# Kernel tuning notes

Measured on AMD Instinct MI355X. Metric: run time of the kernel, lower is better.

## Reference

```python
import jax, jax.numpy as jnp
import numpy as np

H_DIM = 256
N_HEADS = 8
HALF = H_DIM // 2

def _lin(x, W, b):
    # torch nn.Linear: y = x @ W.T + b
    y = x @ W.T
    return y + b if b is not None else y

def setup_inputs() -> dict:
    key = jax.random.key(0)
    ks = jax.random.split(key, 16)
    s = 0.02
    d = {
        'x': jax.random.normal(ks[0], (16, H_DIM, 32, 32), jnp.float32),
        'q1_w': jax.random.normal(ks[1], (HALF, HALF), jnp.float32) * s,
        'q1_b': jnp.zeros((HALF,), jnp.float32),
        'q2_w': jax.random.normal(ks[2], (HALF, HALF), jnp.float32) * s,
        'q2_b': jnp.zeros((HALF,), jnp.float32),
        'k1_w': jax.random.normal(ks[3], (HALF, HALF), jnp.float32) * s,
        'k1_b': jnp.zeros((HALF,), jnp.float32),
        'k2_w': jax.random.normal(ks[4], (HALF, HALF), jnp.float32) * s,
        'k2_b': jnp.zeros((HALF,), jnp.float32),
        'v1_w': jax.random.normal(ks[5], (HALF, HALF), jnp.float32) * s,
        'v1_b': jnp.zeros((HALF,), jnp.float32),
        'v2_w': jax.random.normal(ks[6], (HALF, HALF), jnp.float32) * s,
        'v2_b': jnp.zeros((HALF,), jnp.float32),
        'proj1_w': jax.random.normal(ks[7], (HALF, HALF), jnp.float32) * s,
        'proj1_b': jnp.zeros((HALF,), jnp.float32),
        'proj2_w': jax.random.normal(ks[8], (HALF, HALF), jnp.float32) * s,
        'proj2_b': jnp.zeros((HALF,), jnp.float32),
        'logit_scale': jnp.log(10.0 * jnp.ones((N_HEADS, 1, 1), jnp.float32)),
        'mlp_w1': jax.random.normal(ks[9], (128, 2), jnp.float32) * s,
        'mlp_b1': jnp.zeros((128,), jnp.float32),
        'mlp_w2': jax.random.normal(ks[10], (N_HEADS, 128), jnp.float32) * s,
    }
    return d

def _rel_pos_index(h, w):
    # static (numpy) relative position index, shape [N, N]
    ch, cw = np.meshgrid(np.arange(h), np.arange(w), indexing='ij')
    coords = np.stack([ch.reshape(-1), cw.reshape(-1)])  # [2, N]
    rel = coords[:, :, None] - coords[:, None, :]         # [2, N, N]
    rel = rel.transpose(1, 2, 0)
    rel[:, :, 0] += h - 1
    rel[:, :, 1] += w - 1
    return rel[:, :, 0] * (2 * w - 1) + rel[:, :, 1]

def _forward(x, q1_w, q1_b, q2_w, q2_b, k1_w, k1_b, k2_w, k2_b,
             v1_w, v1_b, v2_w, v2_b, proj1_w, proj1_b, proj2_w, proj2_b,
             logit_scale, mlp_w1, mlp_b1, mlp_w2):
    b, c, h, w = x.shape
    N = h * w
    nh = N_HEADS
    hd = c // nh
    x3 = jnp.transpose(x, (0, 2, 3, 1)).reshape(b, N, c)
    x0, x1 = x3[..., :c // 2], x3[..., c // 2:]

    def qkv(W0, b0, W1, b1):
        t = jnp.concatenate([x0 + _lin(x0, W0, b0), x1 + _lin(x1, W1, b1)], axis=-1)
        return t.reshape(b, N, nh, hd).transpose(0, 2, 1, 3)  # [b, nh, N, hd]

    q = qkv(q1_w, q1_b, q2_w, q2_b)
    k = qkv(k1_w, k1_b, k2_w, k2_b)
    v = qkv(v1_w, v1_b, v2_w, v2_b)

    eps = 1e-12
    qn = q / jnp.maximum(jnp.linalg.norm(q, axis=-1, keepdims=True), eps)
    kn = k / jnp.maximum(jnp.linalg.norm(k, axis=-1, keepdims=True), eps)
    attn = jnp.einsum('bhnd,bhmd->bhnm', qn, kn)  # cosine similarity
    scale = jnp.exp(jnp.minimum(logit_scale, jnp.log(1.0 / 0.01)))  # [nh,1,1]
    attn = attn * scale[None]

    # continuous relative-position bias (CPB) table via small MLP
    rch = jnp.arange(-(h - 1), h, dtype=jnp.float32) / (h - 1 + 1e-8)
    rcw = jnp.arange(-(w - 1), w, dtype=jnp.float32) / (w - 1 + 1e-8)
    gh, gw = jnp.meshgrid(rch, rcw, indexing='ij')
    tab = jnp.stack([gh, gw], axis=-1) * 3.2               # [2h-1, 2w-1, 2]
    tab = jnp.sign(tab) * (1.0 - jnp.exp(-jnp.abs(tab)))
    tab = jax.nn.relu(_lin(tab, mlp_w1, mlp_b1))
    tab = _lin(tab, mlp_w2, None).reshape(-1, nh)          # [(2h-1)(2w-1), nh]

    idx = jnp.asarray(_rel_pos_index(h, w))                # [N, N]
    bias = tab[idx.reshape(-1)].reshape(N, N, nh).transpose(2, 0, 1)
    bias = 16.0 * jax.nn.sigmoid(bias)
    attn = attn + bias[None]

    attn = jax.nn.softmax(attn, axis=-1)
    out = jnp.einsum('bhnm,bhmd->bhnd', attn, v).transpose(0, 2, 1, 3).reshape(b, N, c)
    o0, o1 = out[..., :c // 2], out[..., c // 2:]
    out = jnp.concatenate([_lin(o0, proj1_w, proj1_b), _lin(o1, proj2_w, proj2_b)], axis=-1)
    return out.reshape(b, h, w, c).transpose(0, 3, 1, 2)

def reference(x, q1_w, q1_b, q2_w, q2_b, k1_w, k1_b, k2_w, k2_b,
              v1_w, v1_b, v2_w, v2_b, proj1_w, proj1_b, proj2_w, proj2_b,
              logit_scale, mlp_w1, mlp_b1, mlp_w2):
    return _forward(x, q1_w, q1_b, q2_w, q2_b, k1_w, k1_b, k2_w, k2_b,
                    v1_w, v1_b, v2_w, v2_b, proj1_w, proj1_b, proj2_w, proj2_b,
                    logit_scale, mlp_w1, mlp_b1, mlp_w2)
```

## Files before the change

kernel.cpp:

```cpp
#include <hip/hip_runtime.h>
#include <cmath>


typedef _Float16 half_t;
typedef __attribute__((ext_vector_type(2))) __fp16 fp16x2;
typedef __attribute__((ext_vector_type(4))) _Float16 half4;
typedef __attribute__((ext_vector_type(8))) _Float16 half8;
typedef __attribute__((ext_vector_type(2))) float float2v;
typedef __attribute__((ext_vector_type(4))) float float4v;
typedef __attribute__((ext_vector_type(4))) unsigned int uint4v;

static __device__ __forceinline__ float4v mfma16(half8 a, half8 b, float4v c) {
  return __builtin_amdgcn_mfma_f32_16x16x32_f16(a, b, c, 0, 0, 0);
}

struct PtrArr8 { const float* p[8]; };

__global__ __launch_bounds__(256) void prep_all(
    PtrArr8 wsrc, PtrArr8 bsrc, half_t* __restrict__ wf,
    float* __restrict__ bws, const float* __restrict__ w1,
    const float* __restrict__ b1, const float* __restrict__ w2,
    const float* __restrict__ ls, float* __restrict__ tabd) {
  __shared__ float smem[1408];
  int blk = blockIdx.x;
  int t = threadIdx.x;
  if (blk < 128) {
    int y = blk >> 4, xx = blk & 15;
    const float* src = nullptr;
    const float* bs = nullptr;
#pragma unroll
    for (int i = 0; i < 8; i++)
      if (i == y) { src = wsrc.p[i]; bs = bsrc.p[i]; }
    int flat = (xx * 256 + t) * 4;
    float4 w = *(const float4*)(src + flat);
    int j = flat >> 7, k = flat & 127;
    if (y < 6) {
      if (k == j)     w.x += 1.0f;
      if (k + 1 == j) w.y += 1.0f;
      if (k + 2 == j) w.z += 1.0f;
      if (k + 3 == j) w.w += 1.0f;
    }
    half4 h;
    h[0] = (half_t)w.x;
    h[1] = (half_t)w.y;
    h[2] = (half_t)w.z;
    h[3] = (half_t)w.w;
    int ng = j >> 4, l = j & 15, ks = k >> 5, quad = (k >> 3) & 3, o8 = k & 7;
    *(half4*)(wf + y * 16384 + ((ng * 4 + ks) * 64 + quad * 16 + l) * 8 +
              o8) = h;
    if (xx == 0 && t < 128) bws[y * 128 + t] = bs[t];
  } else {
    float* sw1 = smem;
    float* sb1 = smem + 256;
    float* sw2 = smem + 384;
    sw1[t] = w1[t];
    if (t < 128) sb1[t] = b1[t];
    for (int i = t; i < 1024; i += 256) sw2[i] = w2[i];
    __syncthreads();
    int p = (blk - 128) * 256 + t;
    if (p >= 3969) return;
    int ph = p / 63, pw = p % 63;
    float t0 = (float)(ph - 31) * (3.2f / 31.0f);
    float t1 = (float)(pw - 31) * (3.2f / 31.0f);
    t0 = copysignf(1.0f - __expf(-fabsf(t0)), t0);
    t1 = copysignf(1.0f - __expf(-fabsf(t1)), t1);
    float acc[8];
#pragma unroll
    for (int hh = 0; hh < 8; hh++) acc[hh] = 0.0f;
    for (int j = 0; j < 128; j++) {
      float hj = fmaxf(0.0f, t0 * sw1[2 * j] + t1 * sw1[2 * j + 1] + sb1[j]);
#pragma unroll
      for (int hh = 0; hh < 8; hh++) acc[hh] += hj * sw2[hh * 128 + j];
    }
    const float L2E = 1.44269504f;
#pragma unroll
    for (int hh = 0; hh < 8; hh++) {
      float scale = __expf(fminf(ls[hh], 4.6051702f));
      float c14 = 14.0f - (scale + 16.0f) * L2E;
      float bias = 16.0f / (1.0f + __expf(-acc[hh]));
      float v = bias * L2E + c14;
      float* td = tabd + hh * 7940;
      td[p * 2 + 1] = v;
      td[p * 2 + 2] = v;
      if (p == 0) td[0] = 0.0f;
    }
  }
}

__global__ __launch_bounds__(256, 4) void qkv_mfma(
    const float* __restrict__ x, const half_t* __restrict__ wfrag,
    const float* __restrict__ lscale, const float* __restrict__ bws,
    half_t* __restrict__ qf, half_t* __restrict__ kf,
    half_t* __restrict__ vf) {
  __shared__ half_t tbuf[4608];
  int t = threadIdx.x;
  int lane = t & 63, wv = t >> 6, l = lane & 15, quad = lane >> 4;
  int rw = wv & 1, cw = wv >> 1;
  int hf = blockIdx.y;
  int m0 = blockIdx.x * 32;
  int b = m0 >> 10, n0 = m0 & 1023;

  {
    const float* xb = x + ((size_t)b * 256 + hf * 128) * 1024 + n0;
    int ch = t >> 3, no = (t & 7) * 4;
#pragma unroll
    for (int p = 0; p < 4; p++) {
      float4 v = *(const float4*)(xb + (size_t)(p * 32 + ch) * 1024 + no);
      half4 h;
      h[0] = (half_t)v.x;
      h[1] = (half_t)v.y;
      h[2] = (half_t)v.z;
      h[3] = (half_t)v.w;
      *(half4*)(tbuf + (p * 32 + ch) * 36 + no) = h;
    }
  }
  __syncthreads();

  half8 afr[4];
#pragma unroll
  for (int ks = 0; ks < 4; ks++) {
    half8 a;
#pragma unroll
    for (int j = 0; j < 8; j++)
      a[j] = tbuf[(ks * 32 + quad * 8 + j) * 36 + rw * 16 + l];
    afr[ks] = a;
  }
  __syncthreads();

  for (int op = 0; op < 3; op++) {
    int combo = op * 2 + hf;
    const half_t* wfb = wfrag + combo * 16384;
    float4v acc[4];
#pragma unroll
    for (int ngl = 0; ngl < 4; ngl++) {
      int ng = cw * 4 + ngl;
      float4v c = {0.f, 0.f, 0.f, 0.f};
#pragma unroll
      for (int ks = 0; ks < 4; ks++) {
        half8 bfrag =
            *(const half8*)(wfb + ((ng * 4 + ks) * 64 + lane) * 8);
        c = mfma16(afr[ks], bfrag, c);
      }
      acc[ngl] = c;
    }
#pragma unroll
    for (int ngl = 0; ngl < 4; ngl++) {
      float bb = bws[combo * 128 + (cw * 4 + ngl) * 16 + l];
#pragma unroll
      for (int r2 = 0; r2 < 4; r2++) acc[ngl][r2] += bb;
    }
    if (op < 2) {
#pragma unroll
      for (int hgl = 0; hgl < 2; hgl++) {
        float sc = 1.0f;
        if (op == 0)
          sc = __expf(fminf(lscale[hf * 4 + cw * 2 + hgl], 4.6051702f)) *
               1.44269504f;
#pragma unroll
        for (int r2 = 0; r2 < 4; r2++) {
          float ss = acc[2 * hgl][r2] * acc[2 * hgl][r2] +
                     acc[2 * hgl + 1][r2] * acc[2 * hgl + 1][r2];
          ss += __shfl_xor(ss, 1, 64);
          ss += __shfl_xor(ss, 2, 64);
          ss += __shfl_xor(ss, 4, 64);
          ss += __shfl_xor(ss, 8, 64);
          float rn = sc / fmaxf(sqrtf(ss), 1e-12f);
          acc[2 * hgl][r2] *= rn;
          acc[2 * hgl + 1][r2] *= rn;
        }
      }
#pragma unroll
      for (int ngl = 0; ngl < 4; ngl++)
#pragma unroll
        for (int r2 = 0; r2 < 4; r2++)
          tbuf[(rw * 16 + quad * 4 + r2) * 136 + (cw * 4 + ngl) * 16 + l] =
              (half_t)acc[ngl][r2];
      __syncthreads();
      half_t* dst = (op == 0) ? qf : kf;
#pragma unroll
      for (int i = 0; i < 2; i++) {
        int idx = t + 256 * i;
        int row = idx >> 4, colc = (idx & 15) * 8;
        half8 vv = *(const half8*)(tbuf + row * 136 + colc);
        int head = hf * 4 + (colc >> 5), d = colc & 31;
        *(half8*)(dst + (((size_t)b * 8 + head) * 1024 + n0 + row) * 32 + d) =
            vv;
      }
      __syncthreads();
    } else {
#pragma unroll
      for (int ngl = 0; ngl < 4; ngl++) {
        int col = (cw * 4 + ngl) * 16 + l;
        half4 hv;
#pragma unroll
        for (int r2 = 0; r2 < 4; r2++) hv[r2] = (half_t)acc[ngl][r2];
        *(half4*)(tbuf + col * 36 + rw * 16 + quad * 4) = hv;
      }
      __syncthreads();
      int p64 = (n0 >> 5) & 1;
      int nb64 = n0 & ~63;
#pragma unroll
      for (int i = 0; i < 8; i++) {
        int idx = t + 256 * i;
        int col = idx >> 4, rp = idx & 15;
        unsigned int val = *(const unsigned int*)(tbuf + col * 36 + rp * 2);
        int head = hf * 4 + (col >> 5);
        int d = col & 31;
        int npos = nb64 + ((rp >> 1) & 3) * 16 + (rp & 1) * 8 + p64 * 4 +
                   ((rp >> 3) & 1) * 2;
        *(unsigned int*)((char*)vf +
                         (((((size_t)b * 8 + head) * 32 + d) * 1024) + npos) *
                             2) = val;
      }
    }
  }
}


#define LOADK(kt)                                                           \
  {                                                                         \
    _Pragma("unroll") for (int nt = 0; nt < 4; nt++)                        \
        kfr[nt] = *(const half8*)(kbase + ((kt)*64 + nt * 16 + l) * 32 +    \
                                  quad * 8);                                \
  }

#define LOADV(kt)                                                           \
  {                                                                         \
    _Pragma("unroll") for (int ks = 0; ks < 2; ks++) {                      \
      vv0[ks] = *(const half8*)(vbase + l * 1024 + (kt)*64 + quad * 16 +    \
                                ks * 8);                                    \
      vv1[ks] = *(const half8*)(vbase + (16 + l) * 1024 + (kt)*64 +         \
                                quad * 16 + ks * 8);                        \
    }                                                                       \
  }

#define QK_PHASE(kt, S, SR)                                                 \
  {                                                                         \
    int rowb = (wv + 31 - 2 * (kt)) * 63 + cA + (S)*16;                     \
    _Pragma("unroll") for (int nt = 0; nt < 4; nt++) {                      \
      int base = rowb - (nt >> 1) * 63 - (nt & 1) * 16;                     \
      float2v p0 = sb2d[base];                                              \
      float2v p1 = sb2d[base - 2];                                          \
      float4v c;                                                            \
      c[0] = p0[1];                                                         \
      c[1] = p0[0];                                                         \
      c[2] = p1[1];                                                         \
      c[3] = p1[0];                                                         \
      SR[nt] = mfma16(kfr[nt], qfr[S], c);                                  \
    }                                                                       \
  }

#define EXP_PACK(S, SR)                                                     \
  {                                                                         \
    unsigned int w0[4], w1[4];                                              \
    _Pragma("unroll") for (int nt = 0; nt < 4; nt++) {                      \
      fp16x2 plo = __builtin_amdgcn_cvt_pkrtz(                              \
          __builtin_amdgcn_exp2f(SR[nt][0]),                                \
          __builtin_amdgcn_exp2f(SR[nt][1]));                               \
      fp16x2 phi = __builtin_amdgcn_cvt_pkrtz(                              \
          __builtin_amdgcn_exp2f(SR[nt][2]),                                \
          __builtin_amdgcn_exp2f(SR[nt][3]));                               \
      w0[nt] = __builtin_bit_cast(unsigned int, plo);                       \
      w1[nt] = __builtin_bit_cast(unsigned int, phi);                       \
    }                                                                       \
    uint4v u0 = {w0[0], w0[1], w0[2], w0[3]};                               \
    uint4v u1 = {w1[0], w1[1], w1[2], w1[3]};                               \
    pf##S[0] = __builtin_bit_cast(half8, u0);                               \
    pf##S[1] = __builtin_bit_cast(half8, u1);                               \
  }

#define PV_PHASE(S)                                                         \
  {                                                                         \
    _Pragma("unroll") for (int ks = 0; ks < 2; ks++) {                      \
      o0[S] = mfma16(pf##S[ks], vv0[ks], o0[S]);                            \
      o1[S] = mfma16(pf##S[ks], vv1[ks], o1[S]);                            \
      accl[S] = mfma16(pf##S[ks], ones, accl[S]);                           \
    }                                                                       \
  }

__global__ __launch_bounds__(256) void attn_mfma(
    const half_t* __restrict__ qf, const half_t* __restrict__ kf,
    const half_t* __restrict__ vf, const float* __restrict__ tabd,
    half_t* __restrict__ ao) {
  __shared__ float2v sb2d[2205];

  int id = blockIdx.x;
  int qo = id >> 7;
  int bh = id & 127;
  int h = bh & 7, b = bh >> 3;
  int t = threadIdx.x;
  int lane = t & 63, wv = t >> 6, l = lane & 15, quad = lane >> 4;
  size_t bhs = (size_t)b * 8 + h;
  const half_t* kbase = kf + bhs * 1024 * 32;
  const half_t* vbase = vf + bhs * 32 * 1024;
  int row0 = qo * 128 + wv * 32;
  int cA = l + 31 - quad * 4;

  half8 kfr[4], vv0[2], vv1[2], qfr[2], pf0[2], pf1[2];
  LOADK(0);
  LOADV(0);
#pragma unroll
  for (int s = 0; s < 2; s++)
    qfr[s] = *(const half8*)(qf + (bhs * 1024 + row0 + s * 16 + l) * 32 +
                             quad * 8);

  {
    const float2v* td =
        (const float2v*)(tabd + (size_t)h * 7940) + qo * 252;
    for (int i = t; i < 2205; i += 256) sb2d[i] = td[i];
  }

  float4v o0[2], o1[2], accl[2];
#pragma unroll
  for (int s = 0; s < 2; s++) {
    o0[s] = (float4v){0.f, 0.f, 0.f, 0.f};
    o1[s] = (float4v){0.f, 0.f, 0.f, 0.f};
    accl[s] = (float4v){0.f, 0.f, 0.f, 0.f};
  }
  half8 ones;
#pragma unroll
  for (int j = 0; j < 8; j++) ones[j] = (half_t)1.0f;

  __syncthreads();

#pragma unroll
  for (int kt = 0; kt < 16; ++kt) {
    float4v sres[4];
    QK_PHASE(kt, 0, sres);
    EXP_PACK(0, sres);
    float4v sres2[4];
    QK_PHASE(kt, 1, sres2);
    if (kt < 15) LOADK(kt + 1);
    EXP_PACK(1, sres2);
    PV_PHASE(0);
    PV_PHASE(1);
    if (kt < 15) LOADV(kt + 1);
  }

#pragma unroll
  for (int s = 0; s < 2; s++) {
#pragma unroll
    for (int r2 = 0; r2 < 4; r2++) {
      float linv = 1.0f / accl[s][r2];
      size_t rowaddr =
          ((size_t)b * 1024 + row0 + s * 16 + quad * 4 + r2) * 256 + h * 32;
      ao[rowaddr + l] = (half_t)(o0[s][r2] * linv);
      ao[rowaddr + 16 + l] = (half_t)(o1[s][r2] * linv);
    }
  }
}

__global__ __launch_bounds__(256, 4) void proj_mfma(
    const half_t* __restrict__ ao, const half_t* __restrict__ wfrag,
    const float* __restrict__ bws, float* __restrict__ out) {
  __shared__ float yt[128 * 36];
  int t = threadIdx.x;
  int lane = t & 63, wv = t >> 6, l = lane & 15, quad = lane >> 4;
  int rw = wv & 1, cw = wv >> 1;
  int hf = blockIdx.y;
  int m0 = blockIdx.x * 32;
  int b = m0 >> 10, n0 = m0 & 1023;

  half8 afr[4];
  const half_t* ab =
      ao + ((size_t)m0 + rw * 16 + l) * 256 + hf * 128 + quad * 8;
#pragma unroll
  for (int ks = 0; ks < 4; ks++) afr[ks] = *(const half8*)(ab + ks * 32);

  const half_t* wfb = wfrag + (6 + hf) * 16384;
#pragma unroll
  for (int ngl = 0; ngl < 4; ngl++) {
    int ng = cw * 4 + ngl;
    float4v c = {0.f, 0.f, 0.f, 0.f};
#pragma unroll
    for (int ks = 0; ks < 4; ks++) {
      half8 bfrag = *(const half8*)(wfb + ((ng * 4 + ks) * 64 + lane) * 8);
      c = mfma16(afr[ks], bfrag, c);
    }
    float bb = bws[(6 + hf) * 128 + ng * 16 + l];
#pragma unroll
    for (int r2 = 0; r2 < 4; r2++) c[r2] += bb;
    *(float4v*)(yt + (ng * 16 + l) * 36 + rw * 16 + quad * 4) = c;
  }
  __syncthreads();
#pragma unroll
  for (int i = 0; i < 4; i++) {
    int idx = t + 256 * i;
    int col = idx >> 3, rg = idx & 7;
    float4v vv = *(const float4v*)(yt + col * 36 + rg * 4);
    *(float4v*)(out + ((size_t)b * 256 + hf * 128 + col) * 1024 + n0 +
                rg * 4) = vv;
  }
}

extern "C" void kernel_launch(void* const* d_in, const int* in_sizes, int n_in,
                              void* d_out, int out_size, void* d_ws,
                              size_t ws_size, hipStream_t stream) {
  (void)in_sizes; (void)n_in; (void)out_size; (void)ws_size;
  const float* x = (const float*)d_in[0];

  half_t* ws = (half_t*)d_ws;
  half_t* qfp = ws;
  half_t* kfp = ws + 4194304;
  half_t* vfp = ws + 8388608;
  half_t* aop = ws + 12582912;
  half_t* wfp = ws + 16777216;
  float* tabd = (float*)((char*)d_ws + 33816576);
  float* bws = (float*)((char*)d_ws + 34070656);

  PtrArr8 wsrc, bsrc;
  const int widx[8] = {1, 3, 5, 7, 9, 11, 13, 15};
  for (int i = 0; i < 8; i++) {
    wsrc.p[i] = (const float*)d_in[widx[i]];
    bsrc.p[i] = (const float*)d_in[widx[i] + 1];
  }

  prep_all<<<144, 256, 0, stream>>>(wsrc, bsrc, wfp, bws,
                                    (const float*)d_in[18],
                                    (const float*)d_in[19],
                                    (const float*)d_in[20],
                                    (const float*)d_in[17], tabd);
  qkv_mfma<<<dim3(512, 2), 256, 0, stream>>>(x, wfp, (const float*)d_in[17],
                                             bws, qfp, kfp, vfp);
  attn_mfma<<<1024, 256, 0, stream>>>(qfp, kfp, vfp, tabd, aop);
  proj_mfma<<<dim3(512, 2), 256, 0, stream>>>(aop, wfp, bws, (float*)d_out);
}
```

Baseline: 189.9 us.

## Fuse all four kernels into one persistent kernel with grid barriers

Merges the weight/bias-table prep, QKV projection, attention and output projection kernels into one 1024-block kernel that separates the stages with software grid-wide barriers built on atomic counters. A memset resets the barrier counter before each launch. The aim is to remove three kernel-launch gaps and their tail effects. It depends on all 1024 blocks being resident at once (256 CUs × 4 blocks), otherwise it deadlocks, and it adds barrier spin time plus the cost of the memset.

After: 702.8 us. 270% more time.

```diff
diff --git a/kernel.cpp b/kernel.cpp
--- a/kernel.cpp
+++ b/kernel.cpp
@@ -14,208 +14,47 @@
   return __builtin_amdgcn_mfma_f32_16x16x32_f16(a, b, c, 0, 0, 0);
 }
 
-struct PtrArr8 { const float* p[8]; };
-
-__global__ __launch_bounds__(256) void prep_all(
-    PtrArr8 wsrc, PtrArr8 bsrc, half_t* __restrict__ wf,
-    float* __restrict__ bws, const float* __restrict__ w1,
-    const float* __restrict__ b1, const float* __restrict__ w2,
-    const float* __restrict__ ls, float* __restrict__ tabd) {
-  __shared__ float smem[1408];
-  int blk = blockIdx.x;
-  int t = threadIdx.x;
-  if (blk < 128) {
-    int y = blk >> 4, xx = blk & 15;
-    const float* src = nullptr;
-    const float* bs = nullptr;
-#pragma unroll
-    for (int i = 0; i < 8; i++)
-      if (i == y) { src = wsrc.p[i]; bs = bsrc.p[i]; }
-    int flat = (xx * 256 + t) * 4;
-    float4 w = *(const float4*)(src + flat);
-    int j = flat >> 7, k = flat & 127;
-    if (y < 6) {
-      if (k == j)     w.x += 1.0f;
-      if (k + 1 == j) w.y += 1.0f;
-      if (k + 2 == j) w.z += 1.0f;
-      if (k + 3 == j) w.w += 1.0f;
-    }
-    half4 h;
-    h[0] = (half_t)w.x;
-    h[1] = (half_t)w.y;
-    h[2] = (half_t)w.z;
-    h[3] = (half_t)w.w;
-    int ng = j >> 4, l = j & 15, ks = k >> 5, quad = (k >> 3) & 3, o8 = k & 7;
-    *(half4*)(wf + y * 16384 + ((ng * 4 + ks) * 64 + quad * 16 + l) * 8 +
-              o8) = h;
-    if (xx == 0 && t < 128) bws[y * 128 + t] = bs[t];
-  } else {
-    float* sw1 = smem;
-    float* sb1 = smem + 256;
-    float* sw2 = smem + 384;
-    sw1[t] = w1[t];
-    if (t < 128) sb1[t] = b1[t];
-    for (int i = t; i < 1024; i += 256) sw2[i] = w2[i];
-    __syncthreads();
-    int p = (blk - 128) * 256 + t;
-    if (p >= 3969) return;
-    int ph = p / 63, pw = p % 63;
-    float t0 = (float)(ph - 31) * (3.2f / 31.0f);
-    float t1 = (float)(pw - 31) * (3.2f / 31.0f);
-    t0 = copysignf(1.0f - __expf(-fabsf(t0)), t0);
-    t1 = copysignf(1.0f - __expf(-fabsf(t1)), t1);
-    float acc[8];
-#pragma unroll
-    for (int hh = 0; hh < 8; hh++) acc[hh] = 0.0f;
-    for (int j = 0; j < 128; j++) {
-      float hj = fmaxf(0.0f, t0 * sw1[2 * j] + t1 * sw1[2 * j + 1] + sb1[j]);
-#pragma unroll
-      for (int hh = 0; hh < 8; hh++) acc[hh] += hj * sw2[hh * 128 + j];
-    }
-    const float L2E = 1.44269504f;
-#pragma unroll
-    for (int hh = 0; hh < 8; hh++) {
-      float scale = __expf(fminf(ls[hh], 4.6051702f));
-      float c14 = 14.0f - (scale + 16.0f) * L2E;
-      float bias = 16.0f / (1.0f + __expf(-acc[hh]));
-      float v = bias * L2E + c14;
-      float* td = tabd + hh * 7940;
-      td[p * 2 + 1] = v;
-      td[p * 2 + 2] = v;
-      if (p == 0) td[0] = 0.0f;
-    }
-  }
+struct FusedArgs {
+  const float* x;
+  const float* wsrc[8];
+  const float* bsrc[8];
+  const float* w1;
+  const float* b1;
+  const float* w2;
+  const float* ls;
+  half_t* wf;
+  float* bws;
+  float* tabd;
+  half_t* qf;
+  half_t* kf;
+  half_t* vf;
+  half_t* ao;
+  float* out;
+  unsigned* bar;
+};
+
+static __device__ __forceinline__ void grid_barrier(unsigned* cnt,
+                                                    unsigned* gen,
+                                                    unsigned nb) {
+  __syncthreads();
+  if (threadIdx.x == 0) {
+    unsigned g =
+        __hip_atomic_load(gen, __ATOMIC_RELAXED, __HIP_MEMORY_SCOPE_AGENT);
+    unsigned prev = __hip_atomic_fetch_add(cnt, 1u, __ATOMIC_ACQ_REL,
+                                           __HIP_MEMORY_SCOPE_AGENT);
+    if (prev == nb - 1u) {
+      __hip_atomic_store(cnt, 0u, __ATOMIC_RELAXED,
+                         __HIP_MEMORY_SCOPE_AGENT);
+      __hip_atomic_fetch_add(gen, 1u, __ATOMIC_ACQ_REL,
+                             __HIP_MEMORY_SCOPE_AGENT);
+    } else {
+      while (__hip_atomic_load(gen, __ATOMIC_ACQUIRE,
+                               __HIP_MEMORY_SCOPE_AGENT) == g)
+        __builtin_amdgcn_s_sleep(8);
+    }
+  }
+  __syncthreads();
 }
-
-__global__ __launch_bounds__(256, 4) void qkv_mfma(
-    const float* __restrict__ x, const half_t* __restrict__ wfrag,
-    const float* __restrict__ lscale, const float* __restrict__ bws,
-    half_t* __restrict__ qf, half_t* __restrict__ kf,
-    half_t* __restrict__ vf) {
-  __shared__ half_t tbuf[4608];
-  int t = threadIdx.x;
-  int lane = t & 63, wv = t >> 6, l = lane & 15, quad = lane >> 4;
-  int rw = wv & 1, cw = wv >> 1;
-  int hf = blockIdx.y;
-  int m0 = blockIdx.x * 32;
-  int b = m0 >> 10, n0 = m0 & 1023;
-
-  {
-    const float* xb = x + ((size_t)b * 256 + hf * 128) * 1024 + n0;
-    int ch = t >> 3, no = (t & 7) * 4;
-#pragma unroll
-    for (int p = 0; p < 4; p++) {
-      float4 v = *(const float4*)(xb + (size_t)(p * 32 + ch) * 1024 + no);
-      half4 h;
-      h[0] = (half_t)v.x;
-      h[1] = (half_t)v.y;
-      h[2] = (half_t)v.z;
-      h[3] = (half_t)v.w;
-      *(half4*)(tbuf + (p * 32 + ch) * 36 + no) = h;
-    }
-  }
-  __syncthreads();
-
-  half8 afr[4];
-#pragma unroll
-  for (int ks = 0; ks < 4; ks++) {
-    half8 a;
-#pragma unroll
-    for (int j = 0; j < 8; j++)
-      a[j] = tbuf[(ks * 32 + quad * 8 + j) * 36 + rw * 16 + l];
-    afr[ks] = a;
-  }
-  __syncthreads();
-
-  for (int op = 0; op < 3; op++) {
-    int combo = op * 2 + hf;
-    const half_t* wfb = wfrag + combo * 16384;
-    float4v acc[4];
-#pragma unroll
-    for (int ngl = 0; ngl < 4; ngl++) {
-      int ng = cw * 4 + ngl;
-      float4v c = {0.f, 0.f, 0.f, 0.f};
-#pragma unroll
-      for (int ks = 0; ks < 4; ks++) {
-        half8 bfrag =
-            *(const half8*)(wfb + ((ng * 4 + ks) * 64 + lane) * 8);
-        c = mfma16(afr[ks], bfrag, c);
-      }
-      acc[ngl] = c;
-    }
-#pragma unroll
-    for (int ngl = 0; ngl < 4; ngl++) {
-      float bb = bws[combo * 128 + (cw * 4 + ngl) * 16 + l];
-#pragma unroll
-      for (int r2 = 0; r2 < 4; r2++) acc[ngl][r2] += bb;
-    }
-    if (op < 2) {
-#pragma unroll
-      for (int hgl = 0; hgl < 2; hgl++) {
-        float sc = 1.0f;
-        if (op == 0)
-          sc = __expf(fminf(lscale[hf * 4 + cw * 2 + hgl], 4.6051702f)) *
-               1.44269504f;
-#pragma unroll
-        for (int r2 = 0; r2 < 4; r2++) {
-          float ss = acc[2 * hgl][r2] * acc[2 * hgl][r2] +
-                     acc[2 * hgl + 1][r2] * acc[2 * hgl + 1][r2];
-          ss += __shfl_xor(ss, 1, 64);
-          ss += __shfl_xor(ss, 2, 64);
-          ss += __shfl_xor(ss, 4, 64);
-          ss += __shfl_xor(ss, 8, 64);
-          float rn = sc / fmaxf(sqrtf(ss), 1e-12f);
-          acc[2 * hgl][r2] *= rn;
-          acc[2 * hgl + 1][r2] *= rn;
-        }
-      }
-#pragma unroll
-      for (int ngl = 0; ngl < 4; ngl++)
-#pragma unroll
-        for (int r2 = 0; r2 < 4; r2++)
-          tbuf[(rw * 16 + quad * 4 + r2) * 136 + (cw * 4 + ngl) * 16 + l] =
-              (half_t)acc[ngl][r2];
-      __syncthreads();
-      half_t* dst = (op == 0) ? qf : kf;
-#pragma unroll
-      for (int i = 0; i < 2; i++) {
-        int idx = t + 256 * i;
-        int row = idx >> 4, colc = (idx & 15) * 8;
-        half8 vv = *(const half8*)(tbuf + row * 136 + colc);
-        int head = hf * 4 + (colc >> 5), d = colc & 31;
-        *(half8*)(dst + (((size_t)b * 8 + head) * 1024 + n0 + row) * 32 + d) =
-            vv;
-      }
-      __syncthreads();
-    } else {
-#pragma unroll
-      for (int ngl = 0; ngl < 4; ngl++) {
-        int col = (cw * 4 + ngl) * 16 + l;
-        half4 hv;
-#pragma unroll
-        for (int r2 = 0; r2 < 4; r2++) hv[r2] = (half_t)acc[ngl][r2];
-        *(half4*)(tbuf + col * 36 + rw * 16 + quad * 4) = hv;
-      }
-      __syncthreads();
-      int p64 = (n0 >> 5) & 1;
-      int nb64 = n0 & ~63;
-#pragma unroll
-      for (int i = 0; i < 8; i++) {
-        int idx = t + 256 * i;
-        int col = idx >> 4, rp = idx & 15;
-        unsigned int val = *(const unsigned int*)(tbuf + col * 36 + rp * 2);
-        int head = hf * 4 + (col >> 5);
-        int d = col & 31;
-        int npos = nb64 + ((rp >> 1) & 3) * 16 + (rp & 1) * 8 + p64 * 4 +
-                   ((rp >> 3) & 1) * 2;
-        *(unsigned int*)((char*)vf +
-                         (((((size_t)b * 8 + head) * 32 + d) * 1024) + npos) *
-                             2) = val;
-      }
-    }
-  }
-}
-
 
 #define LOADK(kt)                                                           \
   {                                                                         \
@@ -278,118 +117,309 @@
     }                                                                       \
   }
 
-__global__ __launch_bounds__(256) void attn_mfma(
-    const half_t* __restrict__ qf, const half_t* __restrict__ kf,
-    const half_t* __restrict__ vf, const float* __restrict__ tabd,
-    half_t* __restrict__ ao) {
-  __shared__ float2v sb2d[2205];
-
+__global__ __launch_bounds__(256, 4) void fused_all(FusedArgs a) {
+  __shared__ float4v smem_raw[1152];
   int id = blockIdx.x;
-  int qo = id >> 7;
-  int bh = id & 127;
-  int h = bh & 7, b = bh >> 3;
   int t = threadIdx.x;
-  int lane = t & 63, wv = t >> 6, l = lane & 15, quad = lane >> 4;
-  size_t bhs = (size_t)b * 8 + h;
-  const half_t* kbase = kf + bhs * 1024 * 32;
-  const half_t* vbase = vf + bhs * 32 * 1024;
-  int row0 = qo * 128 + wv * 32;
-  int cA = l + 31 - quad * 4;
-
-  half8 kfr[4], vv0[2], vv1[2], qfr[2], pf0[2], pf1[2];
-  LOADK(0);
-  LOADV(0);
-#pragma unroll
-  for (int s = 0; s < 2; s++)
-    qfr[s] = *(const half8*)(qf + (bhs * 1024 + row0 + s * 16 + l) * 32 +
-                             quad * 8);
+
+  if (id < 128) {
+    int y = id >> 4, xx = id & 15;
+    const float* src = nullptr;
+    const float* bs = nullptr;
+#pragma unroll
+    for (int i = 0; i < 8; i++)
+      if (i == y) { src = a.wsrc[i]; bs = a.bsrc[i]; }
+    int flat = (xx * 256 + t) * 4;
+    float4 w = *(const float4*)(src + flat);
+    int j = flat >> 7, k = flat & 127;
+    if (y < 6) {
+      if (k == j)     w.x += 1.0f;
+      if (k + 1 == j) w.y += 1.0f;
+      if (k + 2 == j) w.z += 1.0f;
+      if (k + 3 == j) w.w += 1.0f;
+    }
+    half4 h;
+    h[0] = (half_t)w.x;
+    h[1] = (half_t)w.y;
+    h[2] = (half_t)w.z;
+    h[3] = (half_t)w.w;
+    int ng = j >> 4, l = j & 15, ks = k >> 5, quad = (k >> 3) & 3, o8 = k & 7;
+    *(half4*)(a.wf + y * 16384 + ((ng * 4 + ks) * 64 + quad * 16 + l) * 8 +
+              o8) = h;
+    if (xx == 0 && t < 128) a.bws[y * 128 + t] = bs[t];
+  } else if (id < 144) {
+    float* smem = (float*)smem_raw;
+    float* sw1 = smem;
+    float* sb1 = smem + 256;
+    float* sw2 = smem + 384;
+    sw1[t] = a.w1[t];
+    if (t < 128) sb1[t] = a.b1[t];
+    for (int i = t; i < 1024; i += 256) sw2[i] = a.w2[i];
+    __syncthreads();
+    int p = (id - 128) * 256 + t;
+    if (p < 3969) {
+      int ph = p / 63, pw = p % 63;
+      float t0 = (float)(ph - 31) * (3.2f / 31.0f);
+      float t1 = (float)(pw - 31) * (3.2f / 31.0f);
+      t0 = copysignf(1.0f - __expf(-fabsf(t0)), t0);
+      t1 = copysignf(1.0f - __expf(-fabsf(t1)), t1);
+      float acc[8];
+#pragma unroll
+      for (int hh = 0; hh < 8; hh++) acc[hh] = 0.0f;
+      for (int j = 0; j < 128; j++) {
+        float hj =
+            fmaxf(0.0f, t0 * sw1[2 * j] + t1 * sw1[2 * j + 1] + sb1[j]);
+#pragma unroll
+        for (int hh = 0; hh < 8; hh++) acc[hh] += hj * sw2[hh * 128 + j];
+      }
+      const float L2E = 1.44269504f;
+#pragma unroll
+      for (int hh = 0; hh < 8; hh++) {
+        float scale = __expf(fminf(a.ls[hh], 4.6051702f));
+        float c14 = 14.0f - (scale + 16.0f) * L2E;
+        float bias = 16.0f / (1.0f + __expf(-acc[hh]));
+        float v = bias * L2E + c14;
+        float* td = a.tabd + hh * 7940;
+        td[p * 2 + 1] = v;
+        td[p * 2 + 2] = v;
+        if (p == 0) td[0] = 0.0f;
+      }
+    }
+  }
+  grid_barrier(a.bar, a.bar + 1, 1024u);
 
   {
-    const float2v* td =
-        (const float2v*)(tabd + (size_t)h * 7940) + qo * 252;
-    for (int i = t; i < 2205; i += 256) sb2d[i] = td[i];
-  }
-
-  float4v o0[2], o1[2], accl[2];
-#pragma unroll
-  for (int s = 0; s < 2; s++) {
-    o0[s] = (float4v){0.f, 0.f, 0.f, 0.f};
-    o1[s] = (float4v){0.f, 0.f, 0.f, 0.f};
-    accl[s] = (float4v){0.f, 0.f, 0.f, 0.f};
-  }
-  half8 ones;
-#pragma unroll
-  for (int j = 0; j < 8; j++) ones[j] = (half_t)1.0f;
-
-  __syncthreads();
-
-#pragma unroll
-  for (int kt = 0; kt < 16; ++kt) {
-    float4v sres[4];
-    QK_PHASE(kt, 0, sres);
-    EXP_PACK(0, sres);
-    float4v sres2[4];
-    QK_PHASE(kt, 1, sres2);
-    if (kt < 15) LOADK(kt + 1);
-    EXP_PACK(1, sres2);
-    PV_PHASE(0);
-    PV_PHASE(1);
-    if (kt < 15) LOADV(kt + 1);
-  }
-
-#pragma unroll
-  for (int s = 0; s < 2; s++) {
-#pragma unroll
-    for (int r2 = 0; r2 < 4; r2++) {
-      float linv = 1.0f / accl[s][r2];
-      size_t rowaddr =
-          ((size_t)b * 1024 + row0 + s * 16 + quad * 4 + r2) * 256 + h * 32;
-      ao[rowaddr + l] = (half_t)(o0[s][r2] * linv);
-      ao[rowaddr + 16 + l] = (half_t)(o1[s][r2] * linv);
-    }
-  }
-}
-
-__global__ __launch_bounds__(256, 4) void proj_mfma(
-    const half_t* __restrict__ ao, const half_t* __restrict__ wfrag,
-    const float* __restrict__ bws, float* __restrict__ out) {
-  __shared__ float yt[128 * 36];
-  int t = threadIdx.x;
-  int lane = t & 63, wv = t >> 6, l = lane & 15, quad = lane >> 4;
-  int rw = wv & 1, cw = wv >> 1;
-  int hf = blockIdx.y;
-  int m0 = blockIdx.x * 32;
-  int b = m0 >> 10, n0 = m0 & 1023;
-
-  half8 afr[4];
-  const half_t* ab =
-      ao + ((size_t)m0 + rw * 16 + l) * 256 + hf * 128 + quad * 8;
-#pragma unroll
-  for (int ks = 0; ks < 4; ks++) afr[ks] = *(const half8*)(ab + ks * 32);
-
-  const half_t* wfb = wfrag + (6 + hf) * 16384;
-#pragma unroll
-  for (int ngl = 0; ngl < 4; ngl++) {
-    int ng = cw * 4 + ngl;
-    float4v c = {0.f, 0.f, 0.f, 0.f};
+    half_t* tbuf = (half_t*)smem_raw;
+    int bx = id & 511, hf = id >> 9;
+    int lane = t & 63, wv = t >> 6, l = lane & 15, quad = lane >> 4;
+    int rw = wv & 1, cw = wv >> 1;
+    int m0 = bx * 32;
+    int b = m0 >> 10, n0 = m0 & 1023;
+
+    {
+      const float* xb = a.x + ((size_t)b * 256 + hf * 128) * 1024 + n0;
+      int ch = t >> 3, no = (t & 7) * 4;
+#pragma unroll
+      for (int p = 0; p < 4; p++) {
+        float4 v = *(const float4*)(xb + (size_t)(p * 32 + ch) * 1024 + no);
+        half4 h;
+        h[0] = (half_t)v.x;
+        h[1] = (half_t)v.y;
+        h[2] = (half_t)v.z;
+        h[3] = (half_t)v.w;
+        *(half4*)(tbuf + (p * 32 + ch) * 36 + no) = h;
+      }
+    }
+    __syncthreads();
+
+    half8 afr[4];
 #pragma unroll
     for (int ks = 0; ks < 4; ks++) {
-      half8 bfrag = *(const half8*)(wfb + ((ng * 4 + ks) * 64 + lane) * 8);
-      c = mfma16(afr[ks], bfrag, c);
-    }
-    float bb = bws[(6 + hf) * 128 + ng * 16 + l];
-#pragma unroll
-    for (int r2 = 0; r2 < 4; r2++) c[r2] += bb;
-    *(float4v*)(yt + (ng * 16 + l) * 36 + rw * 16 + quad * 4) = c;
-  }
-  __syncthreads();
-#pragma unroll
-  for (int i = 0; i < 4; i++) {
-    int idx = t + 256 * i;
-    int col = idx >> 3, rg = idx & 7;
-    float4v vv = *(const float4v*)(yt + col * 36 + rg * 4);
-    *(float4v*)(out + ((size_t)b * 256 + hf * 128 + col) * 1024 + n0 +
-                rg * 4) = vv;
+      half8 aa;
+#pragma unroll
+      for (int j = 0; j < 8; j++)
+        aa[j] = tbuf[(ks * 32 + quad * 8 + j) * 36 + rw * 16 + l];
+      afr[ks] = aa;
+    }
+    __syncthreads();
+
+    for (int op = 0; op < 3; op++) {
+      int combo = op * 2 + hf;
+      const half_t* wfb = a.wf + combo * 16384;
+      float4v acc[4];
+#pragma unroll
+      for (int ngl = 0; ngl < 4; ngl++) {
+        int ng = cw * 4 + ngl;
+        float4v c = {0.f, 0.f, 0.f, 0.f};
+#pragma unroll
+        for (int ks = 0; ks < 4; ks++) {
+          half8 bfrag =
+              *(const half8*)(wfb + ((ng * 4 + ks) * 64 + lane) * 8);
+          c = mfma16(afr[ks], bfrag, c);
+        }
+        acc[ngl] = c;
+      }
+#pragma unroll
+      for (int ngl = 0; ngl < 4; ngl++) {
+        float bb = a.bws[combo * 128 + (cw * 4 + ngl) * 16 + l];
+#pragma unroll
+        for (int r2 = 0; r2 < 4; r2++) acc[ngl][r2] += bb;
+      }
+      if (op < 2) {
+#pragma unroll
+        for (int hgl = 0; hgl < 2; hgl++) {
+          float sc = 1.0f;
+          if (op == 0)
+            sc = __expf(fminf(a.ls[hf * 4 + cw * 2 + hgl], 4.6051702f)) *
+                 1.44269504f;
+#pragma unroll
+          for (int r2 = 0; r2 < 4; r2++) {
+            float ss = acc[2 * hgl][r2] * acc[2 * hgl][r2] +
+                       acc[2 * hgl + 1][r2] * acc[2 * hgl + 1][r2];
+            ss += __shfl_xor(ss, 1, 64);
+            ss += __shfl_xor(ss, 2, 64);
+            ss += __shfl_xor(ss, 4, 64);
+            ss += __shfl_xor(ss, 8, 64);
+            float rn = sc / fmaxf(sqrtf(ss), 1e-12f);
+            acc[2 * hgl][r2] *= rn;
+            acc[2 * hgl + 1][r2] *= rn;
+          }
+        }
+#pragma unroll
+        for (int ngl = 0; ngl < 4; ngl++)
+#pragma unroll
+          for (int r2 = 0; r2 < 4; r2++)
+            tbuf[(rw * 16 + quad * 4 + r2) * 136 + (cw * 4 + ngl) * 16 + l] =
+                (half_t)acc[ngl][r2];
+        __syncthreads();
+        half_t* dst = (op == 0) ? a.qf : a.kf;
+#pragma unroll
+        for (int i = 0; i < 2; i++) {
+          int idx = t + 256 * i;
+          int row = idx >> 4, colc = (idx & 15) * 8;
+          half8 vv = *(const half8*)(tbuf + row * 136 + colc);
+          int head = hf * 4 + (colc >> 5), d = colc & 31;
+          *(half8*)(dst + (((size_t)b * 8 + head) * 1024 + n0 + row) * 32 +
+                    d) = vv;
+        }
+        __syncthreads();
+      } else {
+#pragma unroll
+        for (int ngl = 0; ngl < 4; ngl++) {
+          int col = (cw * 4 + ngl) * 16 + l;
+          half4 hv;
+#pragma unroll
+          for (int r2 = 0; r2 < 4; r2++) hv[r2] = (half_t)acc[ngl][r2];
+          *(half4*)(tbuf + col * 36 + rw * 16 + quad * 4) = hv;
+        }
+        __syncthreads();
+        int p64 = (n0 >> 5) & 1;
+        int nb64 = n0 & ~63;
+#pragma unroll
+        for (int i = 0; i < 8; i++) {
+          int idx = t + 256 * i;
+          int col = idx >> 4, rp = idx & 15;
+          unsigned int val =
+              *(const unsigned int*)(tbuf + col * 36 + rp * 2);
+          int head = hf * 4 + (col >> 5);
+          int d = col & 31;
+          int npos = nb64 + ((rp >> 1) & 3) * 16 + (rp & 1) * 8 + p64 * 4 +
+                     ((rp >> 3) & 1) * 2;
+          *(unsigned int*)((char*)a.vf +
+                           (((((size_t)b * 8 + head) * 32 + d) * 1024) +
+                            npos) * 2) = val;
+        }
+      }
+    }
+  }
+  grid_barrier(a.bar, a.bar + 1, 1024u);
+
+  {
+    float2v* sb2d = (float2v*)smem_raw;
+    int qo = id >> 7;
+    int bh = id & 127;
+    int h = bh & 7, b = bh >> 3;
+    int lane = t & 63, wv = t >> 6, l = lane & 15, quad = lane >> 4;
+    size_t bhs = (size_t)b * 8 + h;
+    const half_t* kbase = a.kf + bhs * 1024 * 32;
+    const half_t* vbase = a.vf + bhs * 32 * 1024;
+    int row0 = qo * 128 + wv * 32;
+    int cA = l + 31 - quad * 4;
+
+    half8 kfr[4], vv0[2], vv1[2], qfr[2], pf0[2], pf1[2];
+    LOADK(0);
+    LOADV(0);
+#pragma unroll
+    for (int s = 0; s < 2; s++)
+      qfr[s] = *(const half8*)(a.qf + (bhs * 1024 + row0 + s * 16 + l) * 32 +
+                               quad * 8);
+
+    {
+      const float2v* td =
+          (const float2v*)(a.tabd + (size_t)h * 7940) + qo * 252;
+      for (int i = t; i < 2205; i += 256) sb2d[i] = td[i];
+    }
+
+    float4v o0[2], o1[2], accl[2];
+#pragma unroll
+    for (int s = 0; s < 2; s++) {
+      o0[s] = (float4v){0.f, 0.f, 0.f, 0.f};
+      o1[s] = (float4v){0.f, 0.f, 0.f, 0.f};
+      accl[s] = (float4v){0.f, 0.f, 0.f, 0.f};
+    }
+    half8 ones;
+#pragma unroll
+    for (int j = 0; j < 8; j++) ones[j] = (half_t)1.0f;
+
+    __syncthreads();
+
+#pragma unroll
+    for (int kt = 0; kt < 16; ++kt) {
+      float4v sres[4];
+      QK_PHASE(kt, 0, sres);
+      EXP_PACK(0, sres);
+      float4v sres2[4];
+      QK_PHASE(kt, 1, sres2);
+      if (kt < 15) LOADK(kt + 1);
+      EXP_PACK(1, sres2);
+      PV_PHASE(0);
+      PV_PHASE(1);
+      if (kt < 15) LOADV(kt + 1);
+    }
+
+#pragma unroll
+    for (int s = 0; s < 2; s++) {
+#pragma unroll
+      for (int r2 = 0; r2 < 4; r2++) {
+        float linv = 1.0f / accl[s][r2];
+        size_t rowaddr =
+            ((size_t)b * 1024 + row0 + s * 16 + quad * 4 + r2) * 256 +
+            h * 32;
+        a.ao[rowaddr + l] = (half_t)(o0[s][r2] * linv);
+        a.ao[rowaddr + 16 + l] = (half_t)(o1[s][r2] * linv);
+      }
+    }
+  }
+  grid_barrier(a.bar, a.bar + 1, 1024u);
+
+  {
+    float* yt = (float*)smem_raw;
+    int bx = id & 511, hf = id >> 9;
+    int lane = t & 63, wv = t >> 6, l = lane & 15, quad = lane >> 4;
+    int rw = wv & 1, cw = wv >> 1;
+    int m0 = bx * 32;
+    int b = m0 >> 10, n0 = m0 & 1023;
+
+    half8 afr[4];
+    const half_t* ab =
+        a.ao + ((size_t)m0 + rw * 16 + l) * 256 + hf * 128 + quad * 8;
+#pragma unroll
+    for (int ks = 0; ks < 4; ks++) afr[ks] = *(const half8*)(ab + ks * 32);
+
+    const half_t* wfb = a.wf + (6 + hf) * 16384;
+#pragma unroll
+    for (int ngl = 0; ngl < 4; ngl++) {
+      int ng = cw * 4 + ngl;
+      float4v c = {0.f, 0.f, 0.f, 0.f};
+#pragma unroll
+      for (int ks = 0; ks < 4; ks++) {
+        half8 bfrag = *(const half8*)(wfb + ((ng * 4 + ks) * 64 + lane) * 8);
+        c = mfma16(afr[ks], bfrag, c);
+      }
+      float bb = a.bws[(6 + hf) * 128 + ng * 16 + l];
+#pragma unroll
+      for (int r2 = 0; r2 < 4; r2++) c[r2] += bb;
+      *(float4v*)(yt + (ng * 16 + l) * 36 + rw * 16 + quad * 4) = c;
+    }
+    __syncthreads();
+#pragma unroll
+    for (int i = 0; i < 4; i++) {
+      int idx = t + 256 * i;
+      int col = idx >> 3, rg = idx & 7;
+      float4v vv = *(const float4v*)(yt + col * 36 + rg * 4);
+      *(float4v*)(a.out + ((size_t)b * 256 + hf * 128 + col) * 1024 + n0 +
+                  rg * 4) = vv;
+    }
   }
 }
 
@@ -397,31 +427,29 @@
                               void* d_out, int out_size, void* d_ws,
                               size_t ws_size, hipStream_t stream) {
   (void)in_sizes; (void)n_in; (void)out_size; (void)ws_size;
-  const float* x = (const float*)d_in[0];
 
   half_t* ws = (half_t*)d_ws;
-  half_t* qfp = ws;
-  half_t* kfp = ws + 4194304;
-  half_t* vfp = ws + 8388608;
-  half_t* aop = ws + 12582912;
-  half_t* wfp = ws + 16777216;
-  float* tabd = (float*)((char*)d_ws + 33816576);
-  float* bws = (float*)((char*)d_ws + 34070656);
-
-  PtrArr8 wsrc, bsrc;
+  FusedArgs fa;
+  fa.x = (const float*)d_in[0];
   const int widx[8] = {1, 3, 5, 7, 9, 11, 13, 15};
   for (int i = 0; i < 8; i++) {
-    wsrc.p[i] = (const float*)d_in[widx[i]];
-    bsrc.p[i] = (const float*)d_in[widx[i] + 1];
-  }
-
-  prep_all<<<144, 256, 0, stream>>>(wsrc, bsrc, wfp, bws,
-                                    (const float*)d_in[18],
-                                    (const float*)d_in[19],
-                                    (const float*)d_in[20],
-                                    (const float*)d_in[17], tabd);
-  qkv_mfma<<<dim3(512, 2), 256, 0, stream>>>(x, wfp, (const float*)d_in[17],
-                                             bws, qfp, kfp, vfp);
-  attn_mfma<<<1024, 256, 0, stream>>>(qfp, kfp, vfp, tabd, aop);
-  proj_mfma<<<dim3(512, 2), 256, 0, stream>>>(aop, wfp, bws, (float*)d_out);
+    fa.wsrc[i] = (const float*)d_in[widx[i]];
+    fa.bsrc[i] = (const float*)d_in[widx[i] + 1];
+  }
+  fa.ls = (const float*)d_in[17];
+  fa.w1 = (const float*)d_in[18];
+  fa.b1 = (const float*)d_in[19];
+  fa.w2 = (const float*)d_in[20];
+  fa.qf = ws;
+  fa.kf = ws + 4194304;
+  fa.vf = ws + 8388608;
+  fa.ao = ws + 12582912;
+  fa.wf = ws + 16777216;
+  fa.tabd = (float*)((char*)d_ws + 33816576);
+  fa.bws = (float*)((char*)d_ws + 34070656);
+  fa.bar = (unsigned*)((char*)d_ws + 34078720);
+  fa.out = (float*)d_out;
+
+  hipMemsetAsync((void*)fa.bar, 0, 64, stream);
+  fused_all<<<dim3(1024), dim3(256), 0, stream>>>(fa);
 }
```

## Split attention key range across two wave groups with LDS reduction

Applied to the files above, without the earlier changes.

The attention kernel now launches 512 threads per block, and the two groups of four waves each handle half of the key tiles for the same query rows. The partial output and row-sum accumulators are combined through a shared-memory buffer before normalisation and the store. This doubles the number of waves per query block so that more MFMA work is in flight and latency is better hidden. In exchange it adds a barrier, 24 KB of LDS per block and an extra reduction step, and the higher LDS use can lower the number of blocks resident per CU. No max-subtraction is needed when adding the partial sums, since the softmax has no running max.

Measured after the change: 188.4 us. About the same (-0.8%).

```diff
diff --git a/kernel.cpp b/kernel.cpp
--- a/kernel.cpp
+++ b/kernel.cpp
@@ -236,7 +236,7 @@
 
 #define QK_PHASE(kt, S, SR)                                                 \
   {                                                                         \
-    int rowb = (wv + 31 - 2 * (kt)) * 63 + cA + (S)*16;                     \
+    int rowb = (wq + 31 - 2 * (kt)) * 63 + cA + (S)*16;                     \
     _Pragma("unroll") for (int nt = 0; nt < 4; nt++) {                      \
       int base = rowb - (nt >> 1) * 63 - (nt & 1) * 16;                     \
       float2v p0 = sb2d[base];                                              \
@@ -278,11 +278,12 @@
     }                                                                       \
   }
 
-__global__ __launch_bounds__(256) void attn_mfma(
+__global__ __launch_bounds__(512) void attn_mfma(
     const half_t* __restrict__ qf, const half_t* __restrict__ kf,
     const half_t* __restrict__ vf, const float* __restrict__ tabd,
     half_t* __restrict__ ao) {
   __shared__ float2v sb2d[2205];
+  __shared__ float red[24 * 256];
 
   int id = blockIdx.x;
   int qo = id >> 7;
@@ -290,15 +291,17 @@
   int h = bh & 7, b = bh >> 3;
   int t = threadIdx.x;
   int lane = t & 63, wv = t >> 6, l = lane & 15, quad = lane >> 4;
+  int wq = wv & 3, wk = wv >> 2;
   size_t bhs = (size_t)b * 8 + h;
   const half_t* kbase = kf + bhs * 1024 * 32;
   const half_t* vbase = vf + bhs * 32 * 1024;
-  int row0 = qo * 128 + wv * 32;
+  int row0 = qo * 128 + wq * 32;
   int cA = l + 31 - quad * 4;
+  int kt0 = wk * 8;
 
   half8 kfr[4], vv0[2], vv1[2], qfr[2], pf0[2], pf1[2];
-  LOADK(0);
-  LOADV(0);
+  LOADK(kt0);
+  LOADV(kt0);
 #pragma unroll
   for (int s = 0; s < 2; s++)
     qfr[s] = *(const half8*)(qf + (bhs * 1024 + row0 + s * 16 + l) * 32 +
@@ -307,7 +310,7 @@
   {
     const float2v* td =
         (const float2v*)(tabd + (size_t)h * 7940) + qo * 252;
-    for (int i = t; i < 2205; i += 256) sb2d[i] = td[i];
+    for (int i = t; i < 2205; i += 512) sb2d[i] = td[i];
   }
 
   float4v o0[2], o1[2], accl[2];
@@ -324,28 +327,53 @@
   __syncthreads();
 
 #pragma unroll
-  for (int kt = 0; kt < 16; ++kt) {
+  for (int i = 0; i < 8; ++i) {
+    int kt = kt0 + i;
     float4v sres[4];
     QK_PHASE(kt, 0, sres);
     EXP_PACK(0, sres);
     float4v sres2[4];
     QK_PHASE(kt, 1, sres2);
-    if (kt < 15) LOADK(kt + 1);
+    if (i < 7) LOADK(kt + 1);
     EXP_PACK(1, sres2);
     PV_PHASE(0);
     PV_PHASE(1);
-    if (kt < 15) LOADV(kt + 1);
-  }
-
-#pragma unroll
-  for (int s = 0; s < 2; s++) {
-#pragma unroll
-    for (int r2 = 0; r2 < 4; r2++) {
-      float linv = 1.0f / accl[s][r2];
-      size_t rowaddr =
-          ((size_t)b * 1024 + row0 + s * 16 + quad * 4 + r2) * 256 + h * 32;
-      ao[rowaddr + l] = (half_t)(o0[s][r2] * linv);
-      ao[rowaddr + 16 + l] = (half_t)(o1[s][r2] * linv);
+    if (i < 7) LOADV(kt + 1);
+  }
+
+  int rbase = wq * 64 + lane;
+  if (wk == 1) {
+#pragma unroll
+    for (int s = 0; s < 2; s++)
+#pragma unroll
+      for (int r2 = 0; r2 < 4; r2++) {
+        red[(s * 12 + r2) * 256 + rbase] = o0[s][r2];
+        red[(s * 12 + 4 + r2) * 256 + rbase] = o1[s][r2];
+        red[(s * 12 + 8 + r2) * 256 + rbase] = accl[s][r2];
+      }
+  }
+  __syncthreads();
+  if (wk == 0) {
+#pragma unroll
+    for (int s = 0; s < 2; s++) {
+#pragma unroll
+      for (int r2 = 0; r2 < 4; r2++) {
+        o0[s][r2] += red[(s * 12 + r2) * 256 + rbase];
+        o1[s][r2] += red[(s * 12 + 4 + r2) * 256 + rbase];
+        accl[s][r2] += red[(s * 12 + 8 + r2) * 256 + rbase];
+      }
+    }
+#pragma unroll
+    for (int s = 0; s < 2; s++) {
+#pragma unroll
+      for (int r2 = 0; r2 < 4; r2++) {
+        float linv = 1.0f / accl[s][r2];
+        size_t rowaddr =
+            ((size_t)b * 1024 + row0 + s * 16 + quad * 4 + r2) * 256 +
+            h * 32;
+        ao[rowaddr + l] = (half_t)(o0[s][r2] * linv);
+        ao[rowaddr + 16 + l] = (half_t)(o1[s][r2] * linv);
+      }
     }
   }
 }
@@ -422,6 +450,6 @@
                                     (const float*)d_in[17], tabd);
   qkv_mfma<<<dim3(512, 2), 256, 0, stream>>>(x, wfp, (const float*)d_in[17],
                                              bws, qfp, kfp, vfp);
-  attn_mfma<<<1024, 256, 0, stream>>>(qfp, kfp, vfp, tabd, aop);
+  attn_mfma<<<1024, 512, 0, stream>>>(qfp, kfp, vfp, tabd, aop);
   proj_mfma<<<dim3(512, 2), 256, 0, stream>>>(aop, wfp, bws, (float*)d_out);
 }
```
